# Optimization experiments

Measured on AMD Instinct MI355X. Metric: run time of the kernel, lower is better.

Reference implementation:

```python
import jax, jax.numpy as jnp
import numpy as np

B, S, H, TOK = 64, 512, 768, 8   # batch rows, tokens/row, hidden, tokens per sentence
K = (B * S) // TOK               # 4096 sentence segments
NUM_CLASSES = 4


def setup_inputs() -> dict:
    key = jax.random.key(0)
    k0, k1, k2, k3 = jax.random.split(key, 4)
    out = jax.random.normal(k0, (B, S, H), dtype=jnp.float32)
    # each row i holds sentences i*64 .. i*64+63, 8 contiguous tokens each
    sent_ids = (jnp.arange(B * S, dtype=jnp.int64) // TOK).reshape(B, S)
    labels = jax.random.randint(k1, (B, S), 0, NUM_CLASSES, dtype=jnp.int64)
    W1 = jax.random.normal(k2, (2 * H, 512), dtype=jnp.float32) * 0.02
    b1 = jnp.zeros((512,), dtype=jnp.float32)
    W2 = jax.random.normal(k3, (512, NUM_CLASSES), dtype=jnp.float32) * 0.02
    b2 = jnp.zeros((NUM_CLASSES,), dtype=jnp.float32)
    return {"out": out, "W1": W1, "b1": b1, "W2": W2, "b2": b2,
            "labels": labels, "sent_ids": sent_ids}


def _ner_forward(out, W1, b1, W2, b2, labels, sent_ids):
    ids = sent_ids.reshape(-1)                      # [B*S]
    x = out.reshape(-1, H)                          # [B*S, H]
    n = ids.shape[0]
    valid = ids >= 0                                # -1 means padding
    seg = jnp.where(valid, ids, K).astype(jnp.int32)  # route invalid to dummy slot K
    w = valid.astype(out.dtype)

    # masked segment mean of token embeddings (avg_vector)
    counts = jax.ops.segment_sum(w, seg, num_segments=K + 1)[:K]            # [K]
    sums = jax.ops.segment_sum(x * w[:, None], seg, num_segments=K + 1)[:K]  # [K,H]
    seg_mean = sums / jnp.maximum(counts, 1.0)[:, None]

    # build_dict: cls vector of segment k = out[i][0] of LAST row containing k
    row = jnp.arange(n) // S
    cls_row = jax.ops.segment_max(jnp.where(valid, row, -1), seg, num_segments=K + 1)[:K]
    cls_vec = out[jnp.maximum(cls_row, 0), 0]       # [K, H]

    # segment label = labels[mask][0] (first token in flattened order)
    first_idx = jax.ops.segment_min(jnp.where(valid, jnp.arange(n), n), seg,
                                    num_segments=K + 1)[:K]
    seg_label = labels.reshape(-1)[jnp.minimum(first_idx, n - 1)]  # [K]

    feats = jnp.concatenate([cls_vec, seg_mean], axis=1)  # [K, 2H]
    h = jax.nn.relu(feats @ W1 + b1)                      # dropout is identity in eval
    probs = jax.nn.softmax(h @ W2 + b2, axis=1)           # [K, 4]

    # Multiclass_Focal_Loss: gather prob at label, -log, sorted truncated sum
    p = jnp.take_along_axis(probs, seg_label[:, None].astype(jnp.int32), axis=1)[:, 0]
    costs = -jnp.log(p)                                   # [K]
    pos = seg_label > 0
    Npos = jnp.sum(pos)
    neg_costs = jnp.where(seg_label == 0, costs, -jnp.inf)
    sorted_desc = -jnp.sort(-neg_costs)                   # descending
    M = jnp.floor(2.5 * Npos.astype(jnp.float32)).astype(jnp.int32)
    take = (jnp.arange(K) < M) & jnp.isfinite(sorted_desc)
    total = jnp.sum(jnp.where(pos, costs, 0.0)) + jnp.sum(jnp.where(take, sorted_desc, 0.0))
    denom = jnp.floor(3.5 * Npos.astype(jnp.float32))
    return total / denom


def reference(out, W1, b1, W2, b2, labels, sent_ids):
    return _ner_forward(out, W1, b1, W2, b2, labels, sent_ids)
```

## Files before the change

### kernel.cpp

```cpp
#include <hip/hip_runtime.h>
#include <hip/hip_bf16.h>
#include <math.h>

#define SDIM 512
#define HDIM 768
#define TOKN 8
#define KSEG 4096
#define HID 512
#define NCLS 4

typedef __attribute__((ext_vector_type(8))) short short8v;
typedef __attribute__((ext_vector_type(4))) float f32x4;

__device__ __forceinline__ ushort f2bf(float f) {
    union { float f; unsigned u; } x; x.f = f;
    return (ushort)((x.u + 0x7FFFu + ((x.u >> 16) & 1u)) >> 16);
}

__global__ __launch_bounds__(256) void prep_small_k(const float* __restrict__ outp,
                                                    const float* __restrict__ W1,
                                                    ushort* __restrict__ W1t,
                                                    float* __restrict__ clsW,
                                                    float* __restrict__ gaccf,
                                                    unsigned* __restrict__ gcnt) {
    __shared__ __align__(16) char smem[18432];
    int bid = blockIdx.x, tid = threadIdx.x;

    if (bid < 8) {
        ushort (*As)[72] = (ushort(*)[72])smem;
        ushort (*Bs)[72] = (ushort(*)[72])(smem + 9216);
        if (bid == 0) {
            if (tid < 2) gaccf[tid] = 0.f;
            if (tid < 3) gcnt[tid] = 0u;
        }
        int nc = bid * 64;
        int lane = tid & 63, wid = tid >> 6;
        int wm = wid >> 1, wn = wid & 1;
        f32x4 acc[2][2] = {};
        int am = tid >> 2, aq = tid & 3;
        int bk = tid >> 4, bq = tid & 15;
        for (int kt = 0; kt < HDIM; kt += 64) {
#pragma unroll
            for (int i = 0; i < 4; ++i) {
                int k = aq * 16 + i * 4;
                float4 v = *(const float4*)(outp + (size_t)am * SDIM * HDIM + kt + k);
                ushort4 u;
                u.x = f2bf(v.x); u.y = f2bf(v.y); u.z = f2bf(v.z); u.w = f2bf(v.w);
                *(ushort4*)(&As[am][k]) = u;
            }
#pragma unroll
            for (int i = 0; i < 4; ++i) {
                int krow = bk + i * 16;
                int n4 = bq * 4;
                float4 v = *(const float4*)(W1 + (size_t)(kt + krow) * HID + nc + n4);
                Bs[n4 + 0][krow] = f2bf(v.x);
                Bs[n4 + 1][krow] = f2bf(v.y);
                Bs[n4 + 2][krow] = f2bf(v.z);
                Bs[n4 + 3][krow] = f2bf(v.w);
            }
            __syncthreads();
            int row = lane & 15, kc = lane >> 4;
#pragma unroll
            for (int ks = 0; ks < 2; ++ks) {
                int kk = ks * 32 + kc * 8;
                short8v afrag[2], bfrag[2];
#pragma unroll
                for (int f = 0; f < 2; ++f) {
                    afrag[f] = *(const short8v*)(&As[wm * 32 + f * 16 + row][kk]);
                    bfrag[f] = *(const short8v*)(&Bs[wn * 32 + f * 16 + row][kk]);
                }
#pragma unroll
                for (int mf = 0; mf < 2; ++mf)
#pragma unroll
                    for (int nf = 0; nf < 2; ++nf)
                        acc[mf][nf] = __builtin_amdgcn_mfma_f32_16x16x32_bf16(
                            afrag[mf], bfrag[nf], acc[mf][nf], 0, 0, 0);
            }
            __syncthreads();
        }
        int col = lane & 15, rg = lane >> 4;
#pragma unroll
        for (int mf = 0; mf < 2; ++mf)
#pragma unroll
            for (int nf = 0; nf < 2; ++nf) {
                int gn = nc + wn * 32 + nf * 16 + col;
#pragma unroll
                for (int r = 0; r < 4; ++r) {
                    int gm = wm * 32 + mf * 16 + rg * 4 + r;
                    clsW[gm * HID + gn] = acc[mf][nf][r];
                }
            }
    } else {
        float (*tile)[33] = (float(*)[33])smem;
        int idx = bid - 8;
        int k0 = (idx % 24) * 32;
        int n0 = (idx / 24) * 32;
        int tx = tid & 31, ty = tid >> 5;
#pragma unroll
        for (int i = 0; i < 4; ++i) {
            int kl = ty + i * 8;
            tile[kl][tx] = W1[(size_t)(HDIM + k0 + kl) * HID + n0 + tx];
        }
        __syncthreads();
#pragma unroll
        for (int i = 0; i < 4; ++i) {
            int nl = ty + i * 8;
            W1t[(size_t)(n0 + nl) * HDIM + k0 + tx] = f2bf(tile[tx][nl]);
        }
    }
}

#define APAD 776

__global__ __launch_bounds__(512) void seg_gemm_head_k(const float* __restrict__ outp,
                                                       const ushort* __restrict__ W1t,
                                                       const float* __restrict__ clsW,
                                                       const float* __restrict__ b1,
                                                       const float* __restrict__ W2,
                                                       float* __restrict__ logits) {
    __shared__ ushort Am[16][APAD];
    __shared__ float pl[8][16][NCLS];
    int tid = threadIdx.x, bm = blockIdx.x;
    int lane = tid & 63, wid = tid >> 6;

    {
        const float4* ob = (const float4*)outp + (size_t)bm * 16 * (TOKN * HDIM / 4);
#pragma unroll
        for (int i = 0; i < 6; ++i) {
            int o = tid + i * 512;
            int s = o / 192, c = o % 192;
            const float4* base = ob + (size_t)s * (TOKN * HDIM / 4) + c;
            float x = 0.f, y = 0.f, z = 0.f, w = 0.f;
#pragma unroll
            for (int t = 0; t < TOKN; ++t) {
                float4 v = base[t * (HDIM / 4)];
                x += v.x; y += v.y; z += v.z; w += v.w;
            }
            ushort4 u;
            u.x = f2bf(x * 0.125f); u.y = f2bf(y * 0.125f);
            u.z = f2bf(z * 0.125f); u.w = f2bf(w * 0.125f);
            *(ushort4*)(&Am[s][c * 4]) = u;
        }
    }
    __syncthreads();

    int n0 = wid * 64;
    int brow = lane & 15, kc = lane >> 4;
    f32x4 acc[4] = {};
    const ushort* bbase = W1t + (size_t)(n0 + brow) * HDIM + kc * 8;
#pragma unroll
    for (int nf = 0; nf < 4; ++nf) {
        const ushort* bp = bbase + (size_t)nf * 16 * HDIM;
        f32x4 a = {};
#pragma unroll
        for (int kt = 0; kt < 24; ++kt) {
            short8v af = *(const short8v*)(&Am[brow][kt * 32 + kc * 8]);
            short8v bf = *(const short8v*)(bp + kt * 32);
            a = __builtin_amdgcn_mfma_f32_16x16x32_bf16(af, bf, a, 0, 0, 0);
        }
        acc[nf] = a;
    }

    int col = lane & 15, rg = lane >> 4;
    int cgrp = (bm >> 2) * HID;
    float4 w2v[4];
#pragma unroll
    for (int nf = 0; nf < 4; ++nf) {
        int gn = n0 + nf * 16 + col;
        float bb = b1[gn];
        float cw = clsW[cgrp + gn];
        w2v[nf] = *(const float4*)(W2 + gn * 4);
#pragma unroll
        for (int r = 0; r < 4; ++r)
            acc[nf][r] = fmaxf(acc[nf][r] + cw + bb, 0.f);
    }
#pragma unroll
    for (int c = 0; c < NCLS; ++c) {
        float pc[4] = {};
#pragma unroll
        for (int nf = 0; nf < 4; ++nf) {
            float wv = (c == 0) ? w2v[nf].x : (c == 1) ? w2v[nf].y
                     : (c == 2) ? w2v[nf].z : w2v[nf].w;
#pragma unroll
            for (int r = 0; r < 4; ++r)
                pc[r] = fmaf(acc[nf][r], wv, pc[r]);
        }
#pragma unroll
        for (int off = 1; off < 16; off <<= 1)
#pragma unroll
            for (int r = 0; r < 4; ++r)
                pc[r] += __shfl_xor(pc[r], off);
        if (col == 0) {
#pragma unroll
            for (int r = 0; r < 4; ++r)
                pl[wid][rg * 4 + r][c] = pc[r];
        }
    }
    __syncthreads();
    if (tid < 16 * NCLS) {
        int m = tid >> 2, c = tid & 3;
        float s = 0.f;
#pragma unroll
        for (int w = 0; w < 8; ++w) s += pl[w][m][c];
        logits[(size_t)(bm * 16 + m) * NCLS + c] = s;
    }
}

__global__ __launch_bounds__(256) void loss_k(const float* __restrict__ logits,
                                              const float* __restrict__ b2,
                                              const int* __restrict__ labels,
                                              float* __restrict__ gaccf,
                                              unsigned* __restrict__ gcnt,
                                              float* __restrict__ negs,
                                              float* __restrict__ res) {
    __shared__ float s_p[4], s_n[4];
    __shared__ unsigned s_pc[4], s_nc[4];
    __shared__ int s_last;
    int tid = threadIdx.x, bid = blockIdx.x;
    int lane = tid & 63, wid = tid >> 6;
    float b20 = b2[0], b21 = b2[1], b22 = b2[2], b23 = b2[3];

    float psum = 0.f, nsum = 0.f;
    unsigned pcnt = 0, ncnt = 0;
#pragma unroll
    for (int i = 0; i < 2; ++i) {
        int k = bid * 512 + i * 256 + tid;
        float4 lv = *(const float4*)(logits + (size_t)k * NCLS);
        float l0 = lv.x + b20, l1 = lv.y + b21, l2 = lv.z + b22, l3 = lv.w + b23;
        int lb = labels[k * TOKN];
        float mx = fmaxf(fmaxf(l0, l1), fmaxf(l2, l3));
        float se = expf(l0 - mx) + expf(l1 - mx) + expf(l2 - mx) + expf(l3 - mx);
        float ll = (lb == 0) ? l0 : (lb == 1) ? l1 : (lb == 2) ? l2 : l3;
        float ck = logf(se) + mx - ll;
        if (lb > 0) { psum += ck; pcnt++; } else { nsum += ck; ncnt++; }
    }
#pragma unroll
    for (int off = 32; off; off >>= 1) {
        psum += __shfl_down(psum, off);
        nsum += __shfl_down(nsum, off);
        pcnt += __shfl_down(pcnt, off);
        ncnt += __shfl_down(ncnt, off);
    }
    if (lane == 0) { s_p[wid] = psum; s_n[wid] = nsum; s_pc[wid] = pcnt; s_nc[wid] = ncnt; }
    __syncthreads();
    if (tid == 0) {
        float bp = s_p[0] + s_p[1] + s_p[2] + s_p[3];
        float bn = s_n[0] + s_n[1] + s_n[2] + s_n[3];
        unsigned bpc = s_pc[0] + s_pc[1] + s_pc[2] + s_pc[3];
        unsigned bnc = s_nc[0] + s_nc[1] + s_nc[2] + s_nc[3];
        atomicAdd(&gaccf[0], bp);
        atomicAdd(&gaccf[1], bn);
        atomicAdd(&gcnt[0], bpc);
        atomicAdd(&gcnt[1], bnc);
    }
    __threadfence();
    if (tid == 0) {
        unsigned t = atomicAdd(&gcnt[2], 1u);
        s_last = (t == 7) ? 1 : 0;
    }
    __syncthreads();
    if (!s_last) return;
    __threadfence();

    float tp = __hip_atomic_load(&gaccf[0], __ATOMIC_RELAXED, __HIP_MEMORY_SCOPE_AGENT);
    float tn = __hip_atomic_load(&gaccf[1], __ATOMIC_RELAXED, __HIP_MEMORY_SCOPE_AGENT);
    unsigned np = __hip_atomic_load(&gcnt[0], __ATOMIC_RELAXED, __HIP_MEMORY_SCOPE_AGENT);
    unsigned nn = __hip_atomic_load(&gcnt[1], __ATOMIC_RELAXED, __HIP_MEMORY_SCOPE_AGENT);
    int M = (int)floorf(2.5f * (float)np);
    if ((int)nn <= M) {
        if (tid == 0) res[0] = (tp + tn) / floorf(3.5f * (float)np);
        return;
    }

    for (int k = tid; k < KSEG; k += 256) {
        float4 lv = *(const float4*)(logits + (size_t)k * NCLS);
        float l0 = lv.x + b20, l1 = lv.y + b21, l2 = lv.z + b22, l3 = lv.w + b23;
        int lb = labels[k * TOKN];
        float mx = fmaxf(fmaxf(l0, l1), fmaxf(l2, l3));
        float se = expf(l0 - mx) + expf(l1 - mx) + expf(l2 - mx) + expf(l3 - mx);
        float ll = (lb == 0) ? l0 : (lb == 1) ? l1 : (lb == 2) ? l2 : l3;
        float ck = logf(se) + mx - ll;
        negs[k] = (lb == 0) ? ck : -INFINITY;
    }
    __syncthreads();
    for (int kk = 2; kk <= KSEG; kk <<= 1) {
        for (int j = kk >> 1; j > 0; j >>= 1) {
            for (int i = tid; i < KSEG; i += 256) {
                int ixj = i ^ j;
                if (ixj > i) {
                    float a = negs[i], b = negs[ixj];
                    bool up = ((i & kk) == 0);
                    if (up ? (a > b) : (a < b)) { negs[i] = b; negs[ixj] = a; }
                }
            }
            __syncthreads();
        }
    }
    float s = 0.f;
    for (int i = tid; i < M; i += 256) {
        float v = negs[KSEG - 1 - i];
        if (isfinite(v)) s += v;
    }
#pragma unroll
    for (int off = 32; off; off >>= 1) s += __shfl_down(s, off);
    if (lane == 0) s_p[wid] = s;
    __syncthreads();
    if (tid == 0) {
        float t = s_p[0] + s_p[1] + s_p[2] + s_p[3];
        res[0] = (tp + t) / floorf(3.5f * (float)np);
    }
}

extern "C" void kernel_launch(void* const* d_in, const int* in_sizes, int n_in,
                              void* d_out, int out_size, void* d_ws, size_t ws_size,
                              hipStream_t stream) {
    const float* outp   = (const float*)d_in[0];
    const float* W1     = (const float*)d_in[1];
    const float* b1     = (const float*)d_in[2];
    const float* W2     = (const float*)d_in[3];
    const float* b2     = (const float*)d_in[4];
    const int*   labels = (const int*)d_in[5];

    char* ws = (char*)d_ws;
    ushort*   W1t    = (ushort*)ws;
    float*    clsW   = (float*) (ws + 786432);
    float*    logits = (float*) (ws + 917504);
    float*    negs   = (float*) (ws + 983040);
    float*    gaccf  = (float*) (ws + 999424);
    unsigned* gcnt   = (unsigned*)(ws + 999432);
    float*    res    = (float*)d_out;

    prep_small_k<<<392, 256, 0, stream>>>(outp, W1, W1t, clsW, gaccf, gcnt);
    seg_gemm_head_k<<<256, 512, 0, stream>>>(outp, W1t, clsW, b1, W2, logits);
    loss_k<<<8, 256, 0, stream>>>(logits, b2, labels, gaccf, gcnt, negs, res);
}
```

Before: 65.94 us.

## Stream segment tokens via double-buffered global_load_lds and halve rows per block

The segment-mean stage now uses direct global-to-LDS loads into two buffers, prefetching the next segment while the current one is reduced, instead of plain register loads. Each block handles 8 segments instead of 16 and the grid doubles to 512 blocks, with a launch-bounds occupancy hint. The MFMA loop is reordered so each A fragment is reused across four B fragments, though half of the 16 MFMA rows now duplicate data and that work is discarded. The intent is to hide HBM latency and raise parallelism, at the cost of redundant matrix work, larger LDS use and more barriers.

```diff
diff --git a/kernel.cpp b/kernel.cpp
--- a/kernel.cpp
+++ b/kernel.cpp
@@ -15,6 +15,12 @@
 __device__ __forceinline__ ushort f2bf(float f) {
     union { float f; unsigned u; } x; x.f = f;
     return (ushort)((x.u + 0x7FFFu + ((x.u >> 16) & 1u)) >> 16);
+}
+
+__device__ __forceinline__ void gload16(const void* g, void* l) {
+    __builtin_amdgcn_global_load_lds(
+        (const __attribute__((address_space(1))) void*)g,
+        (__attribute__((address_space(3))) void*)l, 16, 0, 0);
 }
 
 __global__ __launch_bounds__(256) void prep_small_k(const float* __restrict__ outp,
@@ -110,69 +116,84 @@
     }
 }
 
-#define APAD 776
-
-__global__ __launch_bounds__(512) void seg_gemm_head_k(const float* __restrict__ outp,
-                                                       const ushort* __restrict__ W1t,
-                                                       const float* __restrict__ clsW,
-                                                       const float* __restrict__ b1,
-                                                       const float* __restrict__ W2,
-                                                       float* __restrict__ logits) {
-    __shared__ ushort Am[16][APAD];
-    __shared__ float pl[8][16][NCLS];
+__global__ __launch_bounds__(512, 4) void seg_gemm_head_k(const float* __restrict__ outp,
+                                                          const ushort* __restrict__ W1t,
+                                                          const float* __restrict__ clsW,
+                                                          const float* __restrict__ b1,
+                                                          const float* __restrict__ W2,
+                                                          float* __restrict__ logits) {
+    __shared__ __align__(16) char smem[62592];
+    ushort* Am = (ushort*)smem;
+    char* buf0 = smem + 12416;
+    char* buf1 = smem + 36992;
+    float* pl  = (float*)(smem + 61568);
+
     int tid = threadIdx.x, bm = blockIdx.x;
     int lane = tid & 63, wid = tid >> 6;
+    const char* gseg = (const char*)outp + (size_t)bm * 8 * 24576 + wid * 3072 + lane * 16;
 
     {
-        const float4* ob = (const float4*)outp + (size_t)bm * 16 * (TOKN * HDIM / 4);
-#pragma unroll
-        for (int i = 0; i < 6; ++i) {
-            int o = tid + i * 512;
-            int s = o / 192, c = o % 192;
-            const float4* base = ob + (size_t)s * (TOKN * HDIM / 4) + c;
-            float x = 0.f, y = 0.f, z = 0.f, w = 0.f;
-#pragma unroll
-            for (int t = 0; t < TOKN; ++t) {
-                float4 v = base[t * (HDIM / 4)];
-                x += v.x; y += v.y; z += v.z; w += v.w;
-            }
-            ushort4 u;
-            u.x = f2bf(x * 0.125f); u.y = f2bf(y * 0.125f);
-            u.z = f2bf(z * 0.125f); u.w = f2bf(w * 0.125f);
-            *(ushort4*)(&Am[s][c * 4]) = u;
-        }
-    }
-    __syncthreads();
+#pragma unroll
+        for (int j = 0; j < 3; ++j)
+            gload16(gseg + j * 1024, buf0 + wid * 3072 + j * 1024);
+
+        for (int c = 0; c < 8; ++c) {
+            char* cur = (c & 1) ? buf1 : buf0;
+            char* nxt = (c & 1) ? buf0 : buf1;
+            if (c < 7) {
+#pragma unroll
+                for (int j = 0; j < 3; ++j)
+                    gload16(gseg + (size_t)(c + 1) * 24576 + j * 1024,
+                            nxt + wid * 3072 + j * 1024);
+                asm volatile("s_waitcnt vmcnt(3)" ::: "memory");
+            } else {
+                asm volatile("s_waitcnt vmcnt(0)" ::: "memory");
+            }
+            __builtin_amdgcn_s_barrier();
+            if (tid < 192) {
+                float x = 0.f, y = 0.f, z = 0.f, w = 0.f;
+#pragma unroll
+                for (int t = 0; t < TOKN; ++t) {
+                    float4 v = *(const float4*)(cur + t * 3072 + tid * 16);
+                    x += v.x; y += v.y; z += v.z; w += v.w;
+                }
+                ushort4 u;
+                u.x = f2bf(x * 0.125f); u.y = f2bf(y * 0.125f);
+                u.z = f2bf(z * 0.125f); u.w = f2bf(w * 0.125f);
+                *(ushort4*)(Am + c * 776 + tid * 4) = u;
+            }
+            asm volatile("s_waitcnt lgkmcnt(0)" ::: "memory");
+            __builtin_amdgcn_s_barrier();
+        }
+    }
 
     int n0 = wid * 64;
     int brow = lane & 15, kc = lane >> 4;
+    int ar = brow & 7;
     f32x4 acc[4] = {};
-    const ushort* bbase = W1t + (size_t)(n0 + brow) * HDIM + kc * 8;
-#pragma unroll
-    for (int nf = 0; nf < 4; ++nf) {
-        const ushort* bp = bbase + (size_t)nf * 16 * HDIM;
-        f32x4 a = {};
-#pragma unroll
-        for (int kt = 0; kt < 24; ++kt) {
-            short8v af = *(const short8v*)(&Am[brow][kt * 32 + kc * 8]);
-            short8v bf = *(const short8v*)(bp + kt * 32);
-            a = __builtin_amdgcn_mfma_f32_16x16x32_bf16(af, bf, a, 0, 0, 0);
-        }
-        acc[nf] = a;
+    const ushort* bb = W1t + (size_t)(n0 + brow) * HDIM + kc * 8;
+    for (int kt = 0; kt < 24; ++kt) {
+        short8v af = *(const short8v*)(Am + ar * 776 + kt * 32 + kc * 8);
+        const ushort* bk = bb + kt * 32;
+#pragma unroll
+        for (int nf = 0; nf < 4; ++nf) {
+            short8v bf = *(const short8v*)(bk + (size_t)nf * 16 * HDIM);
+            acc[nf] = __builtin_amdgcn_mfma_f32_16x16x32_bf16(af, bf, acc[nf], 0, 0, 0);
+        }
     }
 
     int col = lane & 15, rg = lane >> 4;
-    int cgrp = (bm >> 2) * HID;
+    int cgrp = (bm >> 3) * HID;
     float4 w2v[4];
 #pragma unroll
     for (int nf = 0; nf < 4; ++nf) {
         int gn = n0 + nf * 16 + col;
-        float bb = b1[gn];
+        float bbias = b1[gn];
         float cw = clsW[cgrp + gn];
         w2v[nf] = *(const float4*)(W2 + gn * 4);
 #pragma unroll
         for (int r = 0; r < 4; ++r)
-            acc[nf][r] = fmaxf(acc[nf][r] + cw + bb, 0.f);
+            acc[nf][r] = fmaxf(acc[nf][r] + cw + bbias, 0.f);
     }
 #pragma unroll
     for (int c = 0; c < NCLS; ++c) {
@@ -190,19 +211,19 @@
 #pragma unroll
             for (int r = 0; r < 4; ++r)
                 pc[r] += __shfl_xor(pc[r], off);
-        if (col == 0) {
+        if (col == 0 && rg < 2) {
 #pragma unroll
             for (int r = 0; r < 4; ++r)
-                pl[wid][rg * 4 + r][c] = pc[r];
-        }
-    }
-    __syncthreads();
-    if (tid < 16 * NCLS) {
+                pl[(wid * 8 + rg * 4 + r) * NCLS + c] = pc[r];
+        }
+    }
+    __syncthreads();
+    if (tid < 8 * NCLS) {
         int m = tid >> 2, c = tid & 3;
         float s = 0.f;
 #pragma unroll
-        for (int w = 0; w < 8; ++w) s += pl[w][m][c];
-        logits[(size_t)(bm * 16 + m) * NCLS + c] = s;
+        for (int w = 0; w < 8; ++w) s += pl[(w * 8 + m) * NCLS + c];
+        logits[(size_t)(bm * 8 + m) * NCLS + c] = s;
     }
 }
 
@@ -331,6 +352,6 @@
     float*    res    = (float*)d_out;
 
     prep_small_k<<<392, 256, 0, stream>>>(outp, W1, W1t, clsW, gaccf, gcnt);
-    seg_gemm_head_k<<<256, 512, 0, stream>>>(outp, W1t, clsW, b1, W2, logits);
+    seg_gemm_head_k<<<512, 512, 0, stream>>>(outp, W1t, clsW, b1, W2, logits);
     loss_k<<<8, 256, 0, stream>>>(logits, b2, labels, gaccf, gcnt, negs, res);
 }
```

Result: slower. 86.72 us (+31.5%).

## Halve segments per block, widen per-wave N tile, swizzle block order

Applied to the files above, without the earlier changes.

The fused segment-mean + GEMM + head kernel now processes 8 segments per block with 256 threads instead of 16 segments with 512. This doubles the grid to 512 blocks for better occupancy on the many CUs, and each wave covers 128 output columns with the K loop reordered so one A fragment feeds 8 MFMAs. Block indices are swizzled so consecutive blocks map to different rows. Because only 8 of the 16 MFMA rows are real (rows duplicated via brow&7), half the MFMA work is wasted, and B traffic per segment doubles.

```diff
diff --git a/kernel.cpp b/kernel.cpp
--- a/kernel.cpp
+++ b/kernel.cpp
@@ -110,30 +110,29 @@
     }
 }
 
-#define APAD 776
-
-__global__ __launch_bounds__(512) void seg_gemm_head_k(const float* __restrict__ outp,
+__global__ __launch_bounds__(256) void seg_gemm_head_k(const float* __restrict__ outp,
                                                        const ushort* __restrict__ W1t,
                                                        const float* __restrict__ clsW,
                                                        const float* __restrict__ b1,
                                                        const float* __restrict__ W2,
                                                        float* __restrict__ logits) {
-    __shared__ ushort Am[16][APAD];
-    __shared__ float pl[8][16][NCLS];
-    int tid = threadIdx.x, bm = blockIdx.x;
+    __shared__ ushort Am[8][776];
+    __shared__ float pl[4][8][NCLS];
+    int tid = threadIdx.x;
+    int bm = ((blockIdx.x & 7) << 6) + (blockIdx.x >> 3);
     int lane = tid & 63, wid = tid >> 6;
 
     {
-        const float4* ob = (const float4*)outp + (size_t)bm * 16 * (TOKN * HDIM / 4);
+        const float4* ob = (const float4*)outp + (size_t)bm * 8 * 1536;
 #pragma unroll
         for (int i = 0; i < 6; ++i) {
-            int o = tid + i * 512;
+            int o = tid + i * 256;
             int s = o / 192, c = o % 192;
-            const float4* base = ob + (size_t)s * (TOKN * HDIM / 4) + c;
+            const float4* base = ob + (size_t)s * 1536 + c;
             float x = 0.f, y = 0.f, z = 0.f, w = 0.f;
 #pragma unroll
             for (int t = 0; t < TOKN; ++t) {
-                float4 v = base[t * (HDIM / 4)];
+                float4 v = base[t * 192];
                 x += v.x; y += v.y; z += v.z; w += v.w;
             }
             ushort4 u;
@@ -144,41 +143,39 @@
     }
     __syncthreads();
 
-    int n0 = wid * 64;
+    int n0 = wid * 128;
     int brow = lane & 15, kc = lane >> 4;
-    f32x4 acc[4] = {};
-    const ushort* bbase = W1t + (size_t)(n0 + brow) * HDIM + kc * 8;
-#pragma unroll
-    for (int nf = 0; nf < 4; ++nf) {
-        const ushort* bp = bbase + (size_t)nf * 16 * HDIM;
-        f32x4 a = {};
-#pragma unroll
-        for (int kt = 0; kt < 24; ++kt) {
-            short8v af = *(const short8v*)(&Am[brow][kt * 32 + kc * 8]);
-            short8v bf = *(const short8v*)(bp + kt * 32);
-            a = __builtin_amdgcn_mfma_f32_16x16x32_bf16(af, bf, a, 0, 0, 0);
-        }
-        acc[nf] = a;
+    int ar = brow & 7;
+    f32x4 acc[8] = {};
+    const ushort* bb = W1t + (size_t)(n0 + brow) * HDIM + kc * 8;
+    for (int kt = 0; kt < 24; ++kt) {
+        short8v af = *(const short8v*)(&Am[ar][kt * 32 + kc * 8]);
+        const ushort* bk = bb + kt * 32;
+#pragma unroll
+        for (int nf = 0; nf < 8; ++nf) {
+            short8v bf = *(const short8v*)(bk + (size_t)nf * 16 * HDIM);
+            acc[nf] = __builtin_amdgcn_mfma_f32_16x16x32_bf16(af, bf, acc[nf], 0, 0, 0);
+        }
     }
 
     int col = lane & 15, rg = lane >> 4;
-    int cgrp = (bm >> 2) * HID;
-    float4 w2v[4];
-#pragma unroll
-    for (int nf = 0; nf < 4; ++nf) {
+    int cgrp = (bm >> 3) * HID;
+    float4 w2v[8];
+#pragma unroll
+    for (int nf = 0; nf < 8; ++nf) {
         int gn = n0 + nf * 16 + col;
-        float bb = b1[gn];
+        float bbias = b1[gn];
         float cw = clsW[cgrp + gn];
         w2v[nf] = *(const float4*)(W2 + gn * 4);
 #pragma unroll
         for (int r = 0; r < 4; ++r)
-            acc[nf][r] = fmaxf(acc[nf][r] + cw + bb, 0.f);
+            acc[nf][r] = fmaxf(acc[nf][r] + cw + bbias, 0.f);
     }
 #pragma unroll
     for (int c = 0; c < NCLS; ++c) {
         float pc[4] = {};
 #pragma unroll
-        for (int nf = 0; nf < 4; ++nf) {
+        for (int nf = 0; nf < 8; ++nf) {
             float wv = (c == 0) ? w2v[nf].x : (c == 1) ? w2v[nf].y
                      : (c == 2) ? w2v[nf].z : w2v[nf].w;
 #pragma unroll
@@ -190,19 +187,17 @@
 #pragma unroll
             for (int r = 0; r < 4; ++r)
                 pc[r] += __shfl_xor(pc[r], off);
-        if (col == 0) {
+        if (col == 0 && rg < 2) {
 #pragma unroll
             for (int r = 0; r < 4; ++r)
                 pl[wid][rg * 4 + r][c] = pc[r];
         }
     }
     __syncthreads();
-    if (tid < 16 * NCLS) {
+    if (tid < 8 * NCLS) {
         int m = tid >> 2, c = tid & 3;
-        float s = 0.f;
-#pragma unroll
-        for (int w = 0; w < 8; ++w) s += pl[w][m][c];
-        logits[(size_t)(bm * 16 + m) * NCLS + c] = s;
+        float s = pl[0][m][c] + pl[1][m][c] + pl[2][m][c] + pl[3][m][c];
+        logits[(size_t)(bm * 8 + m) * NCLS + c] = s;
     }
 }
 
@@ -331,6 +326,6 @@
     float*    res    = (float*)d_out;
 
     prep_small_k<<<392, 256, 0, stream>>>(outp, W1, W1t, clsW, gaccf, gcnt);
-    seg_gemm_head_k<<<256, 512, 0, stream>>>(outp, W1t, clsW, b1, W2, logits);
+    seg_gemm_head_k<<<512, 256, 0, stream>>>(outp, W1t, clsW, b1, W2, logits);
     loss_k<<<8, 256, 0, stream>>>(logits, b2, labels, gaccf, gcnt, negs, res);
 }
```

Measured after the change: 85.10 us. 29.1% more time.
